# Performance work log

Measured on AMD Instinct MI355X. Metric: run time of the kernel, lower is better.

Reference implementation:

```python
import jax, jax.numpy as jnp
import numpy as np
from jax import lax

NUM_CNNS = 300
INPUT_LEN = 608
NUM_CLASSES = 50
FILTER = 19
POOL = 7
HIDDEN = 100
BATCH = 256
L_CONV = INPUT_LEN - FILTER + 1          # 590
L_POOL = (L_CONV - POOL) // POOL + 1     # 84
EPS = 1e-5


def setup_inputs() -> dict:
    key = jax.random.key(0)
    ks = jax.random.split(key, 24)
    U, H = NUM_CNNS, HIDDEN
    d = {}
    d["x"] = jax.random.normal(ks[0], (BATCH, 4, INPUT_LEN), dtype=jnp.float32)
    # conv1: grouped Conv1d(4*U -> U, k=19, groups=U) on replicated input == dense Conv1d(4 -> U)
    d["w1"] = jax.random.normal(ks[1], (U, 4, FILTER), dtype=jnp.float32) * 0.1
    d["b1"] = jax.random.normal(ks[2], (U,), dtype=jnp.float32) * 0.05
    d["g1"] = jax.random.uniform(ks[3], (U,), dtype=jnp.float32, minval=0.5, maxval=1.5)
    d["be1"] = jax.random.normal(ks[4], (U,), dtype=jnp.float32) * 0.05
    d["m1"] = jax.random.normal(ks[5], (U,), dtype=jnp.float32) * 0.05
    d["v1"] = jax.random.uniform(ks[6], (U,), dtype=jnp.float32, minval=0.5, maxval=1.5)
    # grouped 1x1 conv: per-unit Linear 84 -> 100
    d["w2"] = jax.random.normal(ks[7], (U, H, L_POOL), dtype=jnp.float32) * (1.0 / np.sqrt(L_POOL))
    d["b2"] = jax.random.normal(ks[8], (U, H), dtype=jnp.float32) * 0.05
    d["g2"] = jax.random.uniform(ks[9], (U, H), dtype=jnp.float32, minval=0.5, maxval=1.5)
    d["be2"] = jax.random.normal(ks[10], (U, H), dtype=jnp.float32) * 0.05
    d["m2"] = jax.random.normal(ks[11], (U, H), dtype=jnp.float32) * 0.05
    d["v2"] = jax.random.uniform(ks[12], (U, H), dtype=jnp.float32, minval=0.5, maxval=1.5)
    # grouped 1x1 conv: per-unit Linear 100 -> 1
    d["w3"] = jax.random.normal(ks[13], (U, H), dtype=jnp.float32) * (1.0 / np.sqrt(H))
    d["b3"] = jax.random.normal(ks[14], (U,), dtype=jnp.float32) * 0.05
    d["g3"] = jax.random.uniform(ks[15], (U,), dtype=jnp.float32, minval=0.5, maxval=1.5)
    d["be3"] = jax.random.normal(ks[16], (U,), dtype=jnp.float32) * 0.05
    d["m3"] = jax.random.normal(ks[17], (U,), dtype=jnp.float32) * 0.05
    d["v3"] = jax.random.uniform(ks[18], (U,), dtype=jnp.float32, minval=0.5, maxval=1.5)
    # final Linear(U -> num_classes)
    d["wf"] = jax.random.normal(ks[19], (NUM_CLASSES, U), dtype=jnp.float32) * (1.0 / np.sqrt(U))
    d["bf"] = jax.random.normal(ks[20], (NUM_CLASSES,), dtype=jnp.float32) * 0.05
    return d


def _bn(y, g, be, m, v):
    return (y - m) * (g * lax.rsqrt(v + EPS)) + be


def reference(x, w1, b1, g1, be1, m1, v1, w2, b2, g2, be2, m2, v2,
              w3, b3, g3, be3, m3, v3, wf, bf):
    # conv1 (replicate + grouped conv == dense conv over 4 channels)
    y = lax.conv_general_dilated(x, w1, window_strides=(1,), padding='VALID',
                                 dimension_numbers=('NCH', 'OIH', 'NCH'))  # [B,U,590]
    y = y + b1[None, :, None]
    y = _bn(y, g1[None, :, None], be1[None, :, None], m1[None, :, None], v1[None, :, None])
    y = jnp.exp(y)  # ExpActivation
    # MaxPool1d(7,7): 590 -> 84 (uses first 588 positions)
    B = y.shape[0]
    y = y[:, :, :L_POOL * POOL].reshape(B, NUM_CNNS, L_POOL, POOL).max(axis=-1)  # [B,U,84]
    # per-unit MLP 84 -> 100 (grouped 1x1 conv) + BN + ReLU (dropout is eval-mode identity)
    h = jnp.einsum('buf,uof->buo', y, w2) + b2[None]  # [B,U,100]
    h = _bn(h, g2[None], be2[None], m2[None], v2[None])
    h = jax.nn.relu(h)
    # per-unit 100 -> 1 + BN + ReLU
    z = jnp.einsum('buo,uo->bu', h, w3) + b3[None]  # [B,U]
    z = _bn(z, g3[None], be3[None], m3[None], v3[None])
    z = jax.nn.relu(z)
    # final Linear
    return z @ wf.T + bf
```

## Files before the change

### kernel.cpp

```cpp
#include <hip/hip_runtime.h>
#include <hip/hip_bf16.h>

#define BATCH    256
#define NU       300
#define LIN      608
#define FILT     19
#define LPOOL    84
#define POOL     7
#define HID      100
#define NCLS     50
#define EPS      1e-5f
#define KP       96
#define NP       112
#define LDK      104
#define WROW     104
#define WBROWS   320
#define TCHUNK   112
#define MTN      19
#define BH       128
#define CSTR     116

typedef __attribute__((ext_vector_type(8))) short short8;
typedef __attribute__((ext_vector_type(4))) float float4v;

#define LDS_WAIT() __asm__ __volatile__("s_waitcnt lgkmcnt(0)" ::: "memory")

__device__ __forceinline__ unsigned short f2bf(float f) {
    unsigned u = __float_as_uint(f);
    u += 0x7fffu + ((u >> 16) & 1u);
    return (unsigned short)(u >> 16);
}
__device__ __forceinline__ float bf2f(unsigned short h) {
    return __uint_as_float(((unsigned)h) << 16);
}

__global__ void k_prep(const float* __restrict__ w1, const float* __restrict__ x,
                       const float* __restrict__ b1, const float* __restrict__ g1,
                       const float* __restrict__ be1, const float* __restrict__ m1,
                       const float* __restrict__ v1,
                       unsigned short* __restrict__ Wbh,
                       unsigned short* __restrict__ Wbl,
                       unsigned int* __restrict__ xc,
                       float2* __restrict__ s1c1)
{
    const int idx = blockIdx.x * 256 + threadIdx.x;
    const int NW = WBROWS * WROW;
    if (idx < NW) {
        const int u = idx / WROW, kk = idx - u * WROW;
        float wv = 0.f;
        if (u < NU && kk < 96) {
            const int c = kk / 24, tap = kk - 24 * c;
            if (tap < FILT) wv = w1[(u * 4 + c) * FILT + tap];
        }
        const unsigned short hi = f2bf(wv);
        Wbh[idx] = hi;
        Wbl[idx] = f2bf(wv - bf2f(hi));
    }
    const int j = idx - NW;
    if (j >= 0 && j < BATCH * 4 * LIN) {
        const float xv = x[j];
        const unsigned short hi = f2bf(xv);
        const unsigned short lo = f2bf(xv - bf2f(hi));
        xc[j] = (unsigned)hi | ((unsigned)lo << 16);
    }
    const int j2 = j - BATCH * 4 * LIN;
    if (j2 >= 0 && j2 < MTN * 16) {
        float2 v = {0.f, 0.f};
        if (j2 < NU) {
            const float s = g1[j2] * rsqrtf(v1[j2] + EPS);
            v.x = s;
            v.y = (b1[j2] - m1[j2]) * s + be1[j2];
        }
        s1c1[j2] = v;
    }
}

__global__ __launch_bounds__(256, 3)
void k_conv7d(const unsigned short* __restrict__ Wbh,
              const unsigned short* __restrict__ Wbl,
              const unsigned int* __restrict__ xc,
              const float2* __restrict__ s1c1,
              unsigned short* __restrict__ ypool)
{
    __shared__ __align__(16) unsigned short Bh[TCHUNK * LDK];
    __shared__ __align__(16) float Cs[4][16 * CSTR];

    const int tid = threadIdx.x;
    const int b   = blockIdx.x;
    const int tc  = blockIdx.y;
    const int t0  = TCHUNK * tc;
    const int NT  = (tc == 5) ? 2 : 7;

    for (int i = tid; i < TCHUNK * 12; i += 256) {
        const int trow = i / 12;
        if (trow >= 16 * NT) continue;
        const int rem   = i - 12 * trow;
        const int c     = rem / 3;
        const int third = rem - 3 * c;
        const int kkb   = 24 * c + 8 * third;
        const int tt0   = t0 + trow + 8 * third;
        const unsigned int* src = xc + ((b * 4 + c) * LIN + tt0);

        unsigned int w[8];
        if (third < 2 && tt0 + 8 <= LIN) {
            const uint4 v0 = *(const uint4*)(src);
            const uint4 v1 = *(const uint4*)(src + 4);
            w[0] = v0.x; w[1] = v0.y; w[2] = v0.z; w[3] = v0.w;
            w[4] = v1.x; w[5] = v1.y; w[6] = v1.z; w[7] = v1.w;
        } else {
#pragma unroll
            for (int j = 0; j < 8; ++j) {
                const int tap = 8 * third + j;
                const int tt  = tt0 + j;
                unsigned int v = 0;
                if (tap < FILT && tt < LIN) v = src[j];
                w[j] = v;
            }
        }
        short8 hv;
#pragma unroll
        for (int j = 0; j < 8; ++j) hv[j] = (short)(w[j] & 0xffffu);
        *(short8*)(&Bh[trow * LDK + kkb]) = hv;
    }
    __syncthreads();

    const int lane = tid & 63;
    const int n    = lane & 15;
    const int quad = lane >> 4;
    const int wave = tid >> 6;
    float* Csw = Cs[wave];

    const int ep_p  = lane >> 2;
    const int ep_ul = lane & 3;

    const int jend = 5 * wave + ((wave == 3) ? 4 : 5);
    for (int mt0 = 5 * wave; mt0 < jend; mt0 += 2) {
        const bool two = (mt0 + 1 < jend);

        short8 a0h[3], a0l[3], a1h[3], a1l[3];
        {
            const unsigned short* wrh = Wbh + (size_t)(mt0 * 16 + n) * WROW;
            const unsigned short* wrl = Wbl + (size_t)(mt0 * 16 + n) * WROW;
#pragma unroll
            for (int s = 0; s < 3; ++s) {
                a0h[s] = *(const short8*)(wrh + 32 * s + 8 * quad);
                a0l[s] = *(const short8*)(wrl + 32 * s + 8 * quad);
            }
            const int m1r = two ? (mt0 + 1) : mt0;
            const unsigned short* wrh1 = Wbh + (size_t)(m1r * 16 + n) * WROW;
            const unsigned short* wrl1 = Wbl + (size_t)(m1r * 16 + n) * WROW;
#pragma unroll
            for (int s = 0; s < 3; ++s) {
                a1h[s] = *(const short8*)(wrh1 + 32 * s + 8 * quad);
                a1l[s] = *(const short8*)(wrl1 + 32 * s + 8 * quad);
            }
        }

        float4v acc[2][7];
#pragma unroll
        for (int t2 = 0; t2 < 2; ++t2)
#pragma unroll
            for (int nt = 0; nt < 7; ++nt)
                acc[t2][nt] = (float4v){0.f, 0.f, 0.f, 0.f};

#pragma unroll
        for (int nt = 0; nt < 7; ++nt) {
            if (nt < NT) {
                short8 bhf[3];
#pragma unroll
                for (int s = 0; s < 3; ++s)
                    bhf[s] = *(const short8*)(&Bh[(16 * nt + n) * LDK + 32 * s + 8 * quad]);
#pragma unroll
                for (int s = 0; s < 3; ++s)
                    acc[0][nt] = __builtin_amdgcn_mfma_f32_16x16x32_bf16(
                        bhf[s], a0h[s], acc[0][nt], 0, 0, 0);
#pragma unroll
                for (int s = 0; s < 3; ++s)
                    acc[0][nt] = __builtin_amdgcn_mfma_f32_16x16x32_bf16(
                        bhf[s], a0l[s], acc[0][nt], 0, 0, 0);
                if (two) {
#pragma unroll
                    for (int s = 0; s < 3; ++s)
                        acc[1][nt] = __builtin_amdgcn_mfma_f32_16x16x32_bf16(
                            bhf[s], a1h[s], acc[1][nt], 0, 0, 0);
#pragma unroll
                    for (int s = 0; s < 3; ++s)
                        acc[1][nt] = __builtin_amdgcn_mfma_f32_16x16x32_bf16(
                            bhf[s], a1l[s], acc[1][nt], 0, 0, 0);
                }
            }
        }

#pragma unroll
        for (int t2 = 0; t2 < 2; ++t2) {
            if (t2 == 1 && !two) break;
            const int mt = mt0 + t2;

            LDS_WAIT();
#pragma unroll
            for (int nt = 0; nt < 7; ++nt) {
                if (nt < NT)
                    *(float4v*)(&Csw[n * CSTR + 16 * nt + 4 * quad]) = acc[t2][nt];
            }
            LDS_WAIT();

            const int  pg  = 16 * tc + ep_p;
            const bool act = (pg < LPOOL);
            float mx[4] = {0.f, 0.f, 0.f, 0.f};
            if (act) {
#pragma unroll
                for (int gi = 0; gi < 4; ++gi) {
                    const float* r = &Csw[(4 * gi + ep_ul) * CSTR + 7 * ep_p];
                    float m0 = fmaxf(r[0], r[1]);
                    float m1 = fmaxf(r[2], r[3]);
                    float m2 = fmaxf(r[4], r[5]);
                    m0 = fmaxf(m0, r[6]);
                    mx[gi] = fmaxf(fmaxf(m0, m1), m2);
                }
            }
#pragma unroll
            for (int gi = 0; gi < 4; ++gi) {
                const int uglob = mt * 16 + 4 * gi + ep_ul;
                if (uglob < NU) {
                    unsigned short outv = 0;
                    if (act) {
                        const float2 sc = s1c1[uglob];
                        outv = f2bf(__expf(fmaf(mx[gi], sc.x, sc.y)));
                    }
                    ypool[((size_t)uglob * BATCH + b) * KP + pg] = outv;
                }
            }
        }
    }
}

__global__ __launch_bounds__(256, 3)
void k_mlp(const unsigned short* __restrict__ ypool,
           const float* __restrict__ w2, const float* __restrict__ b2,
           const float* __restrict__ g2, const float* __restrict__ be2,
           const float* __restrict__ m2, const float* __restrict__ v2,
           const float* __restrict__ w3, const float* __restrict__ b3,
           const float* __restrict__ g3, const float* __restrict__ be3,
           const float* __restrict__ m3, const float* __restrict__ v3,
           float* __restrict__ zbuf)
{
    __shared__ __align__(16) unsigned short As[NP * LDK];
    __shared__ __align__(16) unsigned short Bs[BH * LDK];
    __shared__ __align__(16) float4 cs4[NP];

    const int tid = threadIdx.x;
    const int u   = blockIdx.x;
    const int b0  = blockIdx.y * BH;

    {
        const float* src = w2 + (size_t)u * HID * LPOOL;
        for (int c = tid; c < HID * (LPOOL / 4); c += 256) {
            const int o  = c / (LPOOL / 4);
            const int kc = (c % (LPOOL / 4)) * 4;
            const float4 v = *(const float4*)(src + o * LPOOL + kc);
            unsigned short* d = &As[o * LDK + kc];
            d[0] = f2bf(v.x); d[1] = f2bf(v.y); d[2] = f2bf(v.z); d[3] = f2bf(v.w);
        }
        for (int c = tid; c < HID * 6; c += 256) {
            const int o = c / 6, kc = LPOOL + (c % 6) * 2;
            *(unsigned*)(&As[o * LDK + kc]) = 0;
        }
        for (int c = tid; c < (NP - HID) * (KP / 2); c += 256) {
            const int o = HID + c / (KP / 2), kc = (c % (KP / 2)) * 2;
            *(unsigned*)(&As[o * LDK + kc]) = 0;
        }
    }
    {
        const unsigned short* ys = ypool + ((size_t)u * BATCH + b0) * KP;
        for (int c = tid; c < BH * (KP / 8); c += 256) {
            const int n  = c / (KP / 8);
            const int kc = (c % (KP / 8)) * 8;
            *(short8*)(&Bs[n * LDK + kc]) = *(const short8*)(ys + n * KP + kc);
        }
    }
    if (tid < NP) {
        float4 cv = {0.f, 0.f, 0.f, 0.f};
        if (tid < HID) {
            const int uo = u * HID + tid;
            const float s = g2[uo] * rsqrtf(v2[uo] + EPS);
            cv.x = s;
            cv.y = (b2[uo] - m2[uo]) * s + be2[uo];
            cv.z = w3[uo];
        }
        cs4[tid] = cv;
    }
    __syncthreads();

    const int lane = tid & 63;
    const int wave = tid >> 6;
    const int col  = lane & 15;
    const int quad = lane >> 4;

    short8 bf_[2][3];
#pragma unroll
    for (int j = 0; j < 2; ++j) {
        const int brow = 16 * (2 * wave + j) + col;
#pragma unroll
        for (int s = 0; s < 3; ++s)
            bf_[j][s] = *(const short8*)(&Bs[brow * LDK + 32 * s + 8 * quad]);
    }

    float zp0 = 0.f, zp1 = 0.f;
#pragma unroll
    for (int mt = 0; mt < 7; ++mt) {
        short8 af[3];
#pragma unroll
        for (int s = 0; s < 3; ++s)
            af[s] = *(const short8*)(&As[(16 * mt + col) * LDK + 32 * s + 8 * quad]);

        float4v a0 = {0.f, 0.f, 0.f, 0.f}, a1 = {0.f, 0.f, 0.f, 0.f};
#pragma unroll
        for (int s = 0; s < 3; ++s) {
            a0 = __builtin_amdgcn_mfma_f32_16x16x32_bf16(af[s], bf_[0][s], a0, 0, 0, 0);
            a1 = __builtin_amdgcn_mfma_f32_16x16x32_bf16(af[s], bf_[1][s], a1, 0, 0, 0);
        }
#pragma unroll
        for (int r = 0; r < 4; ++r) {
            const float4 cv = cs4[16 * mt + 4 * quad + r];
            zp0 = fmaf(fmaxf(fmaf(a0[r], cv.x, cv.y), 0.f), cv.z, zp0);
            zp1 = fmaf(fmaxf(fmaf(a1[r], cv.x, cv.y), 0.f), cv.z, zp1);
        }
    }

    zp0 += __shfl_xor(zp0, 16); zp0 += __shfl_xor(zp0, 32);
    zp1 += __shfl_xor(zp1, 16); zp1 += __shfl_xor(zp1, 32);

    if (quad == 0) {
        const float s3 = g3[u] * rsqrtf(v3[u] + EPS);
        const float c3 = (b3[u] - m3[u]) * s3 + be3[u];
        const int bA = b0 + 16 * (2 * wave + 0) + col;
        const int bB = b0 + 16 * (2 * wave + 1) + col;
        zbuf[(size_t)u * BATCH + bA] = fmaxf(fmaf(zp0, s3, c3), 0.f);
        zbuf[(size_t)u * BATCH + bB] = fmaxf(fmaf(zp1, s3, c3), 0.f);
    }
}

__global__ __launch_bounds__(256, 4)
void k_final(const float* __restrict__ zbuf, const float* __restrict__ wf,
             const float* __restrict__ bf, float* __restrict__ out)
{
    __shared__ float red[4][64];
    const int nc   = blockIdx.x;
    const int bq   = blockIdx.y;
    const int lane = threadIdx.x & 63;
    const int wave = threadIdx.x >> 6;
    const int b    = bq * 64 + lane;

    float a0 = 0.f, a1 = 0.f, a2 = 0.f;
    const int u0 = wave * 75;
#pragma unroll 5
    for (int i = 0; i < 75; i += 3) {
        a0 = fmaf(zbuf[(size_t)(u0 + i + 0) * BATCH + b], wf[nc * NU + u0 + i + 0], a0);
        a1 = fmaf(zbuf[(size_t)(u0 + i + 1) * BATCH + b], wf[nc * NU + u0 + i + 1], a1);
        a2 = fmaf(zbuf[(size_t)(u0 + i + 2) * BATCH + b], wf[nc * NU + u0 + i + 2], a2);
    }
    red[wave][lane] = (a0 + a1) + a2;
    __syncthreads();
    if (threadIdx.x < 64) {
        const float s = (red[0][lane] + red[1][lane]) + (red[2][lane] + red[3][lane]);
        out[(size_t)b * NCLS + nc] = s + bf[nc];
    }
}

extern "C" void kernel_launch(void* const* d_in, const int* in_sizes, int n_in,
                              void* d_out, int out_size, void* d_ws, size_t ws_size,
                              hipStream_t stream)
{
    const float* x   = (const float*)d_in[0];
    const float* w1  = (const float*)d_in[1];
    const float* b1  = (const float*)d_in[2];
    const float* g1  = (const float*)d_in[3];
    const float* be1 = (const float*)d_in[4];
    const float* m1  = (const float*)d_in[5];
    const float* v1  = (const float*)d_in[6];
    const float* w2  = (const float*)d_in[7];
    const float* b2  = (const float*)d_in[8];
    const float* g2  = (const float*)d_in[9];
    const float* be2 = (const float*)d_in[10];
    const float* m2  = (const float*)d_in[11];
    const float* v2  = (const float*)d_in[12];
    const float* w3  = (const float*)d_in[13];
    const float* b3  = (const float*)d_in[14];
    const float* g3  = (const float*)d_in[15];
    const float* be3 = (const float*)d_in[16];
    const float* m3  = (const float*)d_in[17];
    const float* v3  = (const float*)d_in[18];
    const float* wf  = (const float*)d_in[19];
    const float* bf  = (const float*)d_in[20];

    unsigned short* ypool = (unsigned short*)d_ws;
    float* zbuf = (float*)((char*)d_ws + 14745600);
    unsigned short* Wbh = (unsigned short*)((char*)d_ws + 15052800);
    unsigned short* Wbl = (unsigned short*)((char*)d_ws + 15119360);
    unsigned int*   xc  = (unsigned int*)((char*)d_ws + 15185920);
    float2*         sc1 = (float2*)((char*)d_ws + 17676288);

    const int prep_elems = WBROWS * WROW + BATCH * 4 * LIN + MTN * 16;
    k_prep<<<(prep_elems + 255) / 256, 256, 0, stream>>>(
        w1, x, b1, g1, be1, m1, v1, Wbh, Wbl, xc, sc1);

    dim3 gc(BATCH, 6);
    k_conv7d<<<gc, 256, 0, stream>>>(Wbh, Wbl, xc, sc1, ypool);

    dim3 gm(NU, BATCH / BH);
    k_mlp<<<gm, 256, 0, stream>>>(ypool, w2, b2, g2, be2, m2, v2,
                                  w3, b3, g3, be3, m3, v3, zbuf);

    dim3 gf(NCLS, 4);
    k_final<<<gf, 256, 0, stream>>>(zbuf, wf, bf, (float*)d_out);
}
```

Before: 152.7 us.

## Split conv unit tiles across two grid z-slices and pipeline weight loads

The conv grid gains a z dimension of 2, so each block handles about half of the 19 unit tiles: waves take 2-3 tiles instead of 4-5. The epilogue staging buffer is halved by writing the accumulator in two 8-row halves, and launch bounds rise from 3 to 4 blocks per CU. The next tile's weights are prefetched into registers while the current tile computes, and the first weight load is issued before the input staging loop. The aim is more parallel blocks and higher occupancy to hide latency, at the cost of building the input tile in LDS twice per (batch, chunk).

```diff
diff --git a/kernel.cpp b/kernel.cpp
--- a/kernel.cpp
+++ b/kernel.cpp
@@ -75,7 +75,7 @@
     }
 }
 
-__global__ __launch_bounds__(256, 3)
+__global__ __launch_bounds__(256, 4)
 void k_conv7d(const unsigned short* __restrict__ Wbh,
               const unsigned short* __restrict__ Wbl,
               const unsigned int* __restrict__ xc,
@@ -83,13 +83,93 @@
               unsigned short* __restrict__ ypool)
 {
     __shared__ __align__(16) unsigned short Bh[TCHUNK * LDK];
-    __shared__ __align__(16) float Cs[4][16 * CSTR];
+    __shared__ __align__(16) float Cs[4][8 * CSTR];
 
     const int tid = threadIdx.x;
     const int b   = blockIdx.x;
     const int tc  = blockIdx.y;
+    const int z   = blockIdx.z;
     const int t0  = TCHUNK * tc;
     const int NT  = (tc == 5) ? 2 : 7;
+
+    const int lane = tid & 63;
+    const int n    = lane & 15;
+    const int quad = lane >> 4;
+    const int wave = tid >> 6;
+    float* Csw = Cs[wave];
+
+    const int ep_p  = lane >> 2;
+    const int ep_ul = lane & 3;
+    const int pg    = 16 * tc + ep_p;
+    const bool act  = (pg < LPOOL);
+
+    int ts, cnt;
+    if (z == 0) { ts = (wave < 2) ? 3 * wave : (2 + 2 * wave); cnt = (wave < 2) ? 3 : 2; }
+    else        { ts = (wave == 0) ? 10 : (11 + 2 * wave);     cnt = (wave == 0) ? 3 : 2; }
+
+    auto loadW = [&](short8 (&ah)[3], short8 (&al)[3], int mt) {
+        const unsigned short* wrh = Wbh + (size_t)(mt * 16 + n) * WROW + 8 * quad;
+        const unsigned short* wrl = Wbl + (size_t)(mt * 16 + n) * WROW + 8 * quad;
+#pragma unroll
+        for (int s = 0; s < 3; ++s) {
+            ah[s] = *(const short8*)(wrh + 32 * s);
+            al[s] = *(const short8*)(wrl + 32 * s);
+        }
+    };
+
+    auto compute_tile = [&](short8 (&ah)[3], short8 (&al)[3], int mt) {
+        float4v acc[7];
+#pragma unroll
+        for (int nt = 0; nt < 7; ++nt) acc[nt] = (float4v){0.f, 0.f, 0.f, 0.f};
+#pragma unroll
+        for (int nt = 0; nt < 7; ++nt) {
+            if (nt < NT) {
+                short8 bhf[3];
+#pragma unroll
+                for (int s = 0; s < 3; ++s)
+                    bhf[s] = *(const short8*)(&Bh[(16 * nt + n) * LDK + 32 * s + 8 * quad]);
+#pragma unroll
+                for (int s = 0; s < 3; ++s)
+                    acc[nt] = __builtin_amdgcn_mfma_f32_16x16x32_bf16(
+                        bhf[s], ah[s], acc[nt], 0, 0, 0);
+#pragma unroll
+                for (int s = 0; s < 3; ++s)
+                    acc[nt] = __builtin_amdgcn_mfma_f32_16x16x32_bf16(
+                        bhf[s], al[s], acc[nt], 0, 0, 0);
+            }
+        }
+#pragma unroll
+        for (int h = 0; h < 2; ++h) {
+            LDS_WAIT();
+            if ((n >> 3) == h) {
+#pragma unroll
+                for (int nt = 0; nt < 7; ++nt)
+                    if (nt < NT)
+                        *(float4v*)(&Csw[(n & 7) * CSTR + 16 * nt + 4 * quad]) = acc[nt];
+            }
+            LDS_WAIT();
+#pragma unroll
+            for (int gi = 0; gi < 2; ++gi) {
+                const int uglob = mt * 16 + 8 * h + 4 * gi + ep_ul;
+                unsigned short outv = 0;
+                if (act) {
+                    const float* r = &Csw[(4 * gi + ep_ul) * CSTR + 7 * ep_p];
+                    float m0 = fmaxf(r[0], r[1]);
+                    float m1 = fmaxf(r[2], r[3]);
+                    float m2 = fmaxf(r[4], r[5]);
+                    m0 = fmaxf(m0, r[6]);
+                    const float mx = fmaxf(fmaxf(m0, m1), m2);
+                    const float2 sc = s1c1[uglob < (MTN * 16) ? uglob : 0];
+                    outv = f2bf(__expf(fmaf(mx, sc.x, sc.y)));
+                }
+                if (uglob < NU)
+                    ypool[((size_t)uglob * BATCH + b) * KP + pg] = outv;
+            }
+        }
+    };
+
+    short8 wAh[3], wAl[3], wXh[3], wXl[3];
+    loadW(wAh, wAl, ts);
 
     for (int i = tid; i < TCHUNK * 12; i += 256) {
         const int trow = i / 12;
@@ -124,113 +204,12 @@
     }
     __syncthreads();
 
-    const int lane = tid & 63;
-    const int n    = lane & 15;
-    const int quad = lane >> 4;
-    const int wave = tid >> 6;
-    float* Csw = Cs[wave];
-
-    const int ep_p  = lane >> 2;
-    const int ep_ul = lane & 3;
-
-    const int jend = 5 * wave + ((wave == 3) ? 4 : 5);
-    for (int mt0 = 5 * wave; mt0 < jend; mt0 += 2) {
-        const bool two = (mt0 + 1 < jend);
-
-        short8 a0h[3], a0l[3], a1h[3], a1l[3];
-        {
-            const unsigned short* wrh = Wbh + (size_t)(mt0 * 16 + n) * WROW;
-            const unsigned short* wrl = Wbl + (size_t)(mt0 * 16 + n) * WROW;
-#pragma unroll
-            for (int s = 0; s < 3; ++s) {
-                a0h[s] = *(const short8*)(wrh + 32 * s + 8 * quad);
-                a0l[s] = *(const short8*)(wrl + 32 * s + 8 * quad);
-            }
-            const int m1r = two ? (mt0 + 1) : mt0;
-            const unsigned short* wrh1 = Wbh + (size_t)(m1r * 16 + n) * WROW;
-            const unsigned short* wrl1 = Wbl + (size_t)(m1r * 16 + n) * WROW;
-#pragma unroll
-            for (int s = 0; s < 3; ++s) {
-                a1h[s] = *(const short8*)(wrh1 + 32 * s + 8 * quad);
-                a1l[s] = *(const short8*)(wrl1 + 32 * s + 8 * quad);
-            }
-        }
-
-        float4v acc[2][7];
-#pragma unroll
-        for (int t2 = 0; t2 < 2; ++t2)
-#pragma unroll
-            for (int nt = 0; nt < 7; ++nt)
-                acc[t2][nt] = (float4v){0.f, 0.f, 0.f, 0.f};
-
-#pragma unroll
-        for (int nt = 0; nt < 7; ++nt) {
-            if (nt < NT) {
-                short8 bhf[3];
-#pragma unroll
-                for (int s = 0; s < 3; ++s)
-                    bhf[s] = *(const short8*)(&Bh[(16 * nt + n) * LDK + 32 * s + 8 * quad]);
-#pragma unroll
-                for (int s = 0; s < 3; ++s)
-                    acc[0][nt] = __builtin_amdgcn_mfma_f32_16x16x32_bf16(
-                        bhf[s], a0h[s], acc[0][nt], 0, 0, 0);
-#pragma unroll
-                for (int s = 0; s < 3; ++s)
-                    acc[0][nt] = __builtin_amdgcn_mfma_f32_16x16x32_bf16(
-                        bhf[s], a0l[s], acc[0][nt], 0, 0, 0);
-                if (two) {
-#pragma unroll
-                    for (int s = 0; s < 3; ++s)
-                        acc[1][nt] = __builtin_amdgcn_mfma_f32_16x16x32_bf16(
-                            bhf[s], a1h[s], acc[1][nt], 0, 0, 0);
-#pragma unroll
-                    for (int s = 0; s < 3; ++s)
-                        acc[1][nt] = __builtin_amdgcn_mfma_f32_16x16x32_bf16(
-                            bhf[s], a1l[s], acc[1][nt], 0, 0, 0);
-                }
-            }
-        }
-
-#pragma unroll
-        for (int t2 = 0; t2 < 2; ++t2) {
-            if (t2 == 1 && !two) break;
-            const int mt = mt0 + t2;
-
-            LDS_WAIT();
-#pragma unroll
-            for (int nt = 0; nt < 7; ++nt) {
-                if (nt < NT)
-                    *(float4v*)(&Csw[n * CSTR + 16 * nt + 4 * quad]) = acc[t2][nt];
-            }
-            LDS_WAIT();
-
-            const int  pg  = 16 * tc + ep_p;
-            const bool act = (pg < LPOOL);
-            float mx[4] = {0.f, 0.f, 0.f, 0.f};
-            if (act) {
-#pragma unroll
-                for (int gi = 0; gi < 4; ++gi) {
-                    const float* r = &Csw[(4 * gi + ep_ul) * CSTR + 7 * ep_p];
-                    float m0 = fmaxf(r[0], r[1]);
-                    float m1 = fmaxf(r[2], r[3]);
-                    float m2 = fmaxf(r[4], r[5]);
-                    m0 = fmaxf(m0, r[6]);
-                    mx[gi] = fmaxf(fmaxf(m0, m1), m2);
-                }
-            }
-#pragma unroll
-            for (int gi = 0; gi < 4; ++gi) {
-                const int uglob = mt * 16 + 4 * gi + ep_ul;
-                if (uglob < NU) {
-                    unsigned short outv = 0;
-                    if (act) {
-                        const float2 sc = s1c1[uglob];
-                        outv = f2bf(__expf(fmaf(mx[gi], sc.x, sc.y)));
-                    }
-                    ypool[((size_t)uglob * BATCH + b) * KP + pg] = outv;
-                }
-            }
-        }
+    if (cnt >= 2) loadW(wXh, wXl, ts + 1);
+    compute_tile(wAh, wAl, ts);
+    if (cnt >= 2) {
+        if (cnt >= 3) loadW(wAh, wAl, ts + 2);
+        compute_tile(wXh, wXl, ts + 1);
+        if (cnt >= 3) compute_tile(wAh, wAl, ts + 2);
     }
 }
 
@@ -404,7 +383,7 @@
     k_prep<<<(prep_elems + 255) / 256, 256, 0, stream>>>(
         w1, x, b1, g1, be1, m1, v1, Wbh, Wbl, xc, sc1);
 
-    dim3 gc(BATCH, 6);
+    dim3 gc(BATCH, 6, 2);
     k_conv7d<<<gc, 256, 0, stream>>>(Wbh, Wbl, xc, sc1, ypool);
 
     dim3 gm(NU, BATCH / BH);
```

Result: slower. 155.8 us (+2.0%).

## Vectorize pooled output writes and switch ypool to batch-major layout

Applied to the files above, without the earlier changes.

The conv epilogue now has each lane handle one unit and four consecutive pooled positions. Lanes read their 28 conv values from LDS as float4 vectors and write the four bf16 outputs with one 8-byte store, replacing scattered 2-byte stores. The intermediate ypool layout changes from unit-major to batch-major so these stores land contiguously. The MLP kernel's loads are updated to the new layout, which makes its reads strided by NU*KP per batch row and costs some read coalescing there.

```diff
diff --git a/kernel.cpp b/kernel.cpp
--- a/kernel.cpp
+++ b/kernel.cpp
@@ -22,6 +22,7 @@
 
 typedef __attribute__((ext_vector_type(8))) short short8;
 typedef __attribute__((ext_vector_type(4))) float float4v;
+typedef __attribute__((ext_vector_type(4))) unsigned short us4;
 
 #define LDS_WAIT() __asm__ __volatile__("s_waitcnt lgkmcnt(0)" ::: "memory")
 
@@ -130,8 +131,9 @@
     const int wave = tid >> 6;
     float* Csw = Cs[wave];
 
-    const int ep_p  = lane >> 2;
-    const int ep_ul = lane & 3;
+    const int u_l = lane & 15;
+    const int wq  = lane >> 4;
+    const int pg0 = 16 * tc + 4 * wq;
 
     const int jend = 5 * wave + ((wave == 3) ? 4 : 5);
     for (int mt0 = 5 * wave; mt0 < jend; mt0 += 2) {
@@ -204,32 +206,30 @@
             }
             LDS_WAIT();
 
-            const int  pg  = 16 * tc + ep_p;
-            const bool act = (pg < LPOOL);
-            float mx[4] = {0.f, 0.f, 0.f, 0.f};
-            if (act) {
-#pragma unroll
-                for (int gi = 0; gi < 4; ++gi) {
-                    const float* r = &Csw[(4 * gi + ep_ul) * CSTR + 7 * ep_p];
-                    float m0 = fmaxf(r[0], r[1]);
-                    float m1 = fmaxf(r[2], r[3]);
-                    float m2 = fmaxf(r[4], r[5]);
-                    m0 = fmaxf(m0, r[6]);
-                    mx[gi] = fmaxf(fmaxf(m0, m1), m2);
+            float rv[28];
+#pragma unroll
+            for (int r7 = 0; r7 < 7; ++r7)
+                *(float4v*)(&rv[4 * r7]) =
+                    *(const float4v*)(&Csw[u_l * CSTR + 28 * wq + 4 * r7]);
+
+            const int uglob = mt * 16 + u_l;
+            const float2 sc = s1c1[uglob];
+            us4 pk;
+#pragma unroll
+            for (int w4 = 0; w4 < 4; ++w4) {
+                const int pg = pg0 + w4;
+                unsigned short ov = 0;
+                if (pg < LPOOL) {
+                    float m0 = fmaxf(rv[7 * w4 + 0], rv[7 * w4 + 1]);
+                    float m1 = fmaxf(rv[7 * w4 + 2], rv[7 * w4 + 3]);
+                    float m2 = fmaxf(rv[7 * w4 + 4], rv[7 * w4 + 5]);
+                    m0 = fmaxf(m0, rv[7 * w4 + 6]);
+                    ov = f2bf(__expf(fmaf(fmaxf(fmaxf(m0, m1), m2), sc.x, sc.y)));
                 }
-            }
-#pragma unroll
-            for (int gi = 0; gi < 4; ++gi) {
-                const int uglob = mt * 16 + 4 * gi + ep_ul;
-                if (uglob < NU) {
-                    unsigned short outv = 0;
-                    if (act) {
-                        const float2 sc = s1c1[uglob];
-                        outv = f2bf(__expf(fmaf(mx[gi], sc.x, sc.y)));
-                    }
-                    ypool[((size_t)uglob * BATCH + b) * KP + pg] = outv;
-                }
-            }
+                pk[w4] = ov;
+            }
+            if (uglob < NU)
+                *(us4*)(&ypool[((size_t)b * NU + uglob) * KP + pg0]) = pk;
         }
     }
 }
@@ -271,11 +271,12 @@
         }
     }
     {
-        const unsigned short* ys = ypool + ((size_t)u * BATCH + b0) * KP;
+        const unsigned short* ys = ypool + (size_t)u * KP;
         for (int c = tid; c < BH * (KP / 8); c += 256) {
             const int n  = c / (KP / 8);
             const int kc = (c % (KP / 8)) * 8;
-            *(short8*)(&Bs[n * LDK + kc]) = *(const short8*)(ys + n * KP + kc);
+            *(short8*)(&Bs[n * LDK + kc]) =
+                *(const short8*)(ys + (size_t)(b0 + n) * NU * KP + kc);
         }
     }
     if (tid < NP) {
```

Result: faster. 149.1 us (-2.3%).
